# Performance work log

Hardware: AMD Instinct MI355X
Metric: run time of the kernel (lower is better)

The kernel has to match this reference:

```python
import jax, jax.numpy as jnp
import numpy as np
import math

RIEMANN_ZEROS_IM = (14.134725142, 21.022039639, 25.01085758, 30.424876126, 32.935061588,
    37.586178159, 40.918719012, 43.327073281, 48.005150881, 49.773832478, 52.970321478,
    56.446247697, 59.347044003, 60.831778525, 65.112544048, 67.079810529, 69.546401711,
    72.067157674, 75.704690699, 77.144840069, 79.33737502, 82.910380854, 84.735492981,
    87.425274613, 88.809111208, 92.491899271, 94.651344041, 95.870634228, 98.831194218,
    101.317851006, 103.72553804, 105.446623052)

D_MODEL = 1024
N_HEADS = 16
D_HEAD = D_MODEL // N_HEADS  # 64
N_PAIRS = D_HEAD // 2        # 32

# normalized inverse frequencies: gamma_n / gamma_1, inverted
_gamma = np.asarray(RIEMANN_ZEROS_IM[:N_PAIRS], dtype=np.float32)
INV_FREQ = jnp.asarray(1.0 / (_gamma / _gamma[0]))  # [n_pairs]


def _rotate(x, cos, sin):
    # x: [b,h,n,d_head]; cos/sin: [1,h,n,n_pairs]; interleaved pair rotation
    x1 = x[..., 0::2]
    x2 = x[..., 1::2]
    rx1 = x1 * cos - x2 * sin
    rx2 = x1 * sin + x2 * cos
    return jnp.stack([rx1, rx2], axis=-1).reshape(x.shape)


def setup_inputs() -> dict:
    key = jax.random.key(0)
    k1, k2, k3 = jax.random.split(key, 3)
    b, n = 4, 2048
    x = jax.random.normal(k1, (b, n, D_MODEL), dtype=jnp.float32)
    # torch Linear(d, 3d, bias=False): y = x @ W.T; we store W.T directly
    w_qkv = jax.random.normal(k2, (D_MODEL, 3 * D_MODEL), dtype=jnp.float32) / math.sqrt(D_MODEL)
    w_o = jax.random.normal(k3, (D_MODEL, D_MODEL), dtype=jnp.float32) / math.sqrt(D_MODEL)
    log_scale = jnp.zeros((N_HEADS,), dtype=jnp.float32)
    return {"x": x, "w_qkv": w_qkv, "w_o": w_o, "log_scale": log_scale}


def reference(x, w_qkv, w_o, log_scale):
    b, n, d = x.shape
    qkv = (x @ w_qkv).reshape(b, n, 3, N_HEADS, D_HEAD)
    q, k, v = qkv[:, :, 0], qkv[:, :, 1], qkv[:, :, 2]  # [b,n,h,dh]
    q = q.transpose(0, 2, 1, 3)  # [b,h,n,dh]
    k = k.transpose(0, 2, 1, 3)
    v = v.transpose(0, 2, 1, 3)

    scale = jnp.exp(log_scale)  # [h]
    pos = jnp.arange(n, dtype=jnp.float32)
    # theta: [1,h,n,n_pairs]
    theta = pos[None, None, :, None] * INV_FREQ[None, None, None, :] * scale[None, :, None, None]
    cos, sin = jnp.cos(theta), jnp.sin(theta)
    q = _rotate(q, cos, sin)
    k = _rotate(k, cos, sin)

    scores = jnp.einsum('bhqd,bhkd->bhqk', q, k) / math.sqrt(D_HEAD)
    causal = jnp.tril(jnp.ones((n, n), dtype=bool))
    scores = jnp.where(causal[None, None], scores, -jnp.inf)
    attn = jax.nn.softmax(scores, axis=-1)
    out = jnp.einsum('bhqk,bhkd->bhqd', attn, v)
    out = out.transpose(0, 2, 1, 3).reshape(b, n, d)
    return out @ w_o
```

## Files before the change

### kernel.cpp

```cpp
#include <hip/hip_runtime.h>
#include <hip/hip_bf16.h>

#define B_ 4
#define N_ 2048
#define DM 1024
#define NH 16
#define DH 64

typedef __attribute__((ext_vector_type(8))) __bf16 bf16x8;
typedef __attribute__((ext_vector_type(4))) float f32x4;
typedef __attribute__((ext_vector_type(4))) float float4v;
typedef __attribute__((ext_vector_type(4))) unsigned int uint4v;
typedef __attribute__((ext_vector_type(2))) unsigned int uint2v;
typedef __attribute__((ext_vector_type(4))) unsigned short ushort4v;

__device__ __forceinline__ float bf2f(unsigned short h) {
  union { unsigned int u; float f; } v; v.u = ((unsigned int)h) << 16; return v.f;
}
__device__ __forceinline__ unsigned short f2bf(float f) {
  __bf16 h = (__bf16)f;
  return __builtin_bit_cast(unsigned short, h);
}
__device__ __forceinline__ f32x4 mfma16(bf16x8 a, bf16x8 b, f32x4 c) {
  return __builtin_amdgcn_mfma_f32_16x16x32_bf16(a, b, c, 0, 0, 0);
}
__device__ __forceinline__ void gload_lds16(const void* g, void* l) {
  __builtin_amdgcn_global_load_lds(
      (const __attribute__((address_space(1))) unsigned int*)g,
      (__attribute__((address_space(3))) unsigned int*)l, 16, 0, 0);
}
__device__ __forceinline__ float fexp2(float x) {
  return __builtin_amdgcn_exp2f(x);
}

__constant__ float GAMMA_C[32] = {
  14.134725142f, 21.022039639f, 25.01085758f, 30.424876126f,
  32.935061588f, 37.586178159f, 40.918719012f, 43.327073281f,
  48.005150881f, 49.773832478f, 52.970321478f, 56.446247697f,
  59.347044003f, 60.831778525f, 65.112544048f, 67.079810529f,
  69.546401711f, 72.067157674f, 75.704690699f, 77.144840069f,
  79.33737502f,  82.910380854f, 84.735492981f, 87.425274613f,
  88.809111208f, 92.491899271f, 94.651344041f, 95.870634228f,
  98.831194218f, 101.317851006f, 103.72553804f, 105.446623052f
};

__global__ __launch_bounds__(256) void cast_f32_bf16(
    const float* __restrict__ in, unsigned short* __restrict__ out, int n4) {
  int i = blockIdx.x * 256 + threadIdx.x;
  if (i >= n4) return;
  float4v v = *(const float4v*)&in[(size_t)i * 4];
  ushort4v o;
  o[0] = f2bf(v[0]); o[1] = f2bf(v[1]); o[2] = f2bf(v[2]); o[3] = f2bf(v[3]);
  *(ushort4v*)&out[(size_t)i * 4] = o;
}

__global__ __launch_bounds__(256) void tcast(
    const float* __restrict__ in, unsigned short* __restrict__ out, int K, int N) {
  __shared__ float t[32][33];
  int n0 = blockIdx.x * 32, k0 = blockIdx.y * 32;
  int tx = threadIdx.x, ty = threadIdx.y;
#pragma unroll
  for (int j = 0; j < 4; ++j)
    t[ty + j * 8][tx] = in[(size_t)(k0 + ty + j * 8) * N + n0 + tx];
  __syncthreads();
#pragma unroll
  for (int j = 0; j < 4; ++j)
    out[(size_t)(n0 + ty + j * 8) * K + k0 + tx] = f2bf(t[tx][ty + j * 8]);
}

template <int OUTF32>
__global__ __launch_bounds__(256) void gemm_bt(
    const unsigned short* __restrict__ A, const unsigned short* __restrict__ BT,
    void* __restrict__ C, int M, int N, int K) {
  __shared__ unsigned short As[128 * 32];
  __shared__ unsigned short Bs[128 * 32];
  int tid = threadIdx.x;
  int lane = tid & 63, wid = tid >> 6;
  int wr = wid >> 1, wc = wid & 1;
  int lr = lane & 15, lg = lane >> 4;
  int bm = blockIdx.y * 128, bn = blockIdx.x * 128;
  int srow = lane >> 2, sch = lane & 3;
  f32x4 acc[4][4];
#pragma unroll
  for (int m = 0; m < 4; ++m)
#pragma unroll
    for (int n = 0; n < 4; ++n) acc[m][n] = (f32x4){0.f, 0.f, 0.f, 0.f};

  for (int k0 = 0; k0 < K; k0 += 32) {
    __syncthreads();
#pragma unroll
    for (int it = 0; it < 2; ++it) {
      int rbase = wid * 16 + it * 64;
      gload_lds16(&A[(size_t)(bm + rbase + srow) * K + k0 + sch * 8],
                  &As[rbase * 32]);
      gload_lds16(&BT[(size_t)(bn + rbase + srow) * K + k0 + sch * 8],
                  &Bs[rbase * 32]);
    }
    __syncthreads();
    bf16x8 af[4], bfr[4];
#pragma unroll
    for (int m = 0; m < 4; ++m)
      af[m] = *(const bf16x8*)&As[(wr * 64 + m * 16 + lr) * 32 + lg * 8];
#pragma unroll
    for (int n = 0; n < 4; ++n)
      bfr[n] = *(const bf16x8*)&Bs[(wc * 64 + n * 16 + lr) * 32 + lg * 8];
    __builtin_amdgcn_s_setprio(1);
#pragma unroll
    for (int m = 0; m < 4; ++m)
#pragma unroll
      for (int n = 0; n < 4; ++n)
        acc[m][n] = mfma16(af[m], bfr[n], acc[m][n]);
    __builtin_amdgcn_s_setprio(0);
  }
#pragma unroll
  for (int m = 0; m < 4; ++m)
#pragma unroll
    for (int n = 0; n < 4; ++n) {
      int row = bm + wr * 64 + m * 16 + lg * 4;
      int col = bn + wc * 64 + n * 16 + lr;
#pragma unroll
      for (int r = 0; r < 4; ++r) {
        if (OUTF32)
          ((float*)C)[(size_t)(row + r) * N + col] = acc[m][n][r];
        else
          ((unsigned short*)C)[(size_t)(row + r) * N + col] = f2bf(acc[m][n][r]);
      }
    }
}

__global__ __launch_bounds__(256) void rope_split(
    const unsigned short* __restrict__ qkv, const float* __restrict__ log_scale,
    unsigned short* __restrict__ Qr, unsigned short* __restrict__ Kr,
    unsigned short* __restrict__ Vr) {
  const float SC = 0.125f * 1.44269504089f;
  int t = blockIdx.x * 256 + threadIdx.x;
  int p = t & 31, h = (t >> 5) & 15, n = (t >> 9) & 2047, b = t >> 20;
  float invf = GAMMA_C[0] / GAMMA_C[p];
  float scale = __expf(log_scale[h]);
  float theta = ((float)n * invf) * scale;
  float sn, cs;
  sincosf(theta, &sn, &cs);
  size_t base = (size_t)(b * N_ + n) * (3 * DM) + h * DH + 2 * p;
  unsigned int qu = *(const unsigned int*)&qkv[base];
  unsigned int ku = *(const unsigned int*)&qkv[base + DM];
  unsigned int vu = *(const unsigned int*)&qkv[base + 2 * DM];
  float q1 = bf2f(qu & 0xffffu), q2 = bf2f(qu >> 16);
  float k1 = bf2f(ku & 0xffffu), k2 = bf2f(ku >> 16);
  unsigned int rq = (unsigned int)f2bf((q1 * cs - q2 * sn) * SC) |
                    ((unsigned int)f2bf((q1 * sn + q2 * cs) * SC) << 16);
  unsigned int rk = (unsigned int)f2bf(k1 * cs - k2 * sn) |
                    ((unsigned int)f2bf(k1 * sn + k2 * cs) << 16);
  size_t ob = (size_t)((b * NH + h) * N_ + n) * DH + 2 * p;
  *(unsigned int*)&Qr[ob] = rq;
  *(unsigned int*)&Kr[ob] = rk;
  *(unsigned int*)&Vr[ob] = vu;
}

__global__ __launch_bounds__(256) void attn_fwd(
    const unsigned short* __restrict__ Q, const unsigned short* __restrict__ K,
    const unsigned short* __restrict__ V, unsigned short* __restrict__ AO) {
  int orig = blockIdx.x;
  int wg = (orig & 7) * 128 + (orig >> 3);
  int i = wg & 15;
  int qt = ((wg >> 5) & 1) ? (15 - i) : i;
  int bh = wg >> 4;
  int b = bh >> 4, h = bh & 15;
  int q0 = qt * 128;
  int tid = threadIdx.x;
  int lane = tid & 63, w = tid >> 6;
  int lr = lane & 15, lg = lane >> 4;

  const unsigned short* Qh = Q + (size_t)bh * N_ * DH;
  const unsigned short* Kh = K + (size_t)bh * N_ * DH;
  const unsigned short* Vh = V + (size_t)bh * N_ * DH;

  __shared__ unsigned short Ks[64 * 64];
  __shared__ unsigned short Vt[64 * 64];
  __shared__ unsigned int PsU[4][32][32];

  bf16x8 qf[2][2];
#pragma unroll
  for (int m = 0; m < 2; ++m)
#pragma unroll
    for (int dh = 0; dh < 2; ++dh)
      qf[m][dh] = *(const bf16x8*)
          &Qh[(size_t)(q0 + w * 32 + m * 16 + lr) * DH + dh * 32 + lg * 8];

  f32x4 oacc[2][4];
#pragma unroll
  for (int m = 0; m < 2; ++m)
#pragma unroll
    for (int nb = 0; nb < 4; ++nb) oacc[m][nb] = (f32x4){0.f, 0.f, 0.f, 0.f};
  float mst[2] = {-1e30f, -1e30f};
  float lst[2] = {0.f, 0.f};

  int wkend = q0 + w * 32 + 31;
  int ksup = q0 + 128;
  int vch = tid & 7, vk = tid >> 3;
  int swz = 4 * (lr & 7);

  for (int k0 = 0; k0 < ksup; k0 += 64) {
    __syncthreads();
#pragma unroll
    for (int it = 0; it < 2; ++it) {
      int rbase = w * 8 + it * 32;
      int row = rbase + (lane >> 3);
      int sk = ((row & 7) ^ (row >> 3)) & 7;
      int ch = lane & 7;
      gload_lds16(&Kh[(size_t)(k0 + row) * DH + ((ch ^ sk) * 8)],
                  &Ks[rbase * 64]);
    }
#pragma unroll
    for (int it = 0; it < 2; ++it) {
      int k = vk + it * 32;
      uint4v vv = *(const uint4v*)&Vh[(size_t)(k0 + k) * DH + vch * 8];
      const unsigned short* pv = (const unsigned short*)&vv;
#pragma unroll
      for (int j = 0; j < 8; ++j) {
        int d = vch * 8 + j;
        int sv = (j ^ vch) & 7;
        Vt[d * 64 + (k ^ (sv << 3))] = pv[j];
      }
    }
    __syncthreads();
    if (k0 > wkend) continue;

    f32x4 s[2][4];
    __builtin_amdgcn_s_setprio(1);
#pragma unroll
    for (int nb = 0; nb < 4; ++nb) {
      int key = nb * 16 + lr;
      int sk = ((key & 7) ^ (key >> 3)) & 7;
      bf16x8 kf0 = *(const bf16x8*)&Ks[key * 64 + ((lg ^ sk) * 8)];
      bf16x8 kf1 = *(const bf16x8*)&Ks[key * 64 + (((4 + lg) ^ sk) * 8)];
#pragma unroll
      for (int m = 0; m < 2; ++m) {
        f32x4 z = (f32x4){0.f, 0.f, 0.f, 0.f};
        z = mfma16(kf0, qf[m][0], z);
        z = mfma16(kf1, qf[m][1], z);
        s[m][nb] = z;
      }
    }
    __builtin_amdgcn_s_setprio(0);

    float mx[2];
#pragma unroll
    for (int m = 0; m < 2; ++m) {
      int qm = q0 + w * 32 + m * 16;
      if (k0 + 63 > qm) {
        int q = qm + lr;
#pragma unroll
        for (int nb = 0; nb < 4; ++nb)
#pragma unroll
          for (int r = 0; r < 4; ++r)
            if (k0 + nb * 16 + lg * 4 + r > q) s[m][nb][r] = -1e30f;
      }
      float mx0 = fmaxf(fmaxf(s[m][0][0], s[m][0][1]),
                        fmaxf(s[m][0][2], s[m][0][3]));
      float mx1 = fmaxf(fmaxf(s[m][1][0], s[m][1][1]),
                        fmaxf(s[m][1][2], s[m][1][3]));
      float mx2 = fmaxf(fmaxf(s[m][2][0], s[m][2][1]),
                        fmaxf(s[m][2][2], s[m][2][3]));
      float mx3 = fmaxf(fmaxf(s[m][3][0], s[m][3][1]),
                        fmaxf(s[m][3][2], s[m][3][3]));
      float m01 = fmaxf(fmaxf(mx0, mx1), fmaxf(mx2, mx3));
      m01 = fmaxf(m01, __shfl_xor(m01, 16, 64));
      m01 = fmaxf(m01, __shfl_xor(m01, 32, 64));
      mx[m] = m01;
    }

    if (__any((mx[0] > mst[0] + 8.f) || (mx[1] > mst[1] + 8.f))) {
      float scs[2];
#pragma unroll
      for (int m = 0; m < 2; ++m) {
        float mnew = fmaxf(mst[m], mx[m]);
        float sc = fexp2(mst[m] - mnew);
        mst[m] = mnew;
        lst[m] *= sc;
        scs[m] = sc;
      }
#pragma unroll
      for (int m = 0; m < 2; ++m)
#pragma unroll
        for (int r = 0; r < 4; ++r) {
          float scr = __shfl(scs[m], lg * 4 + r, 64);
#pragma unroll
          for (int nb = 0; nb < 4; ++nb) oacc[m][nb][r] *= scr;
        }
    }

#pragma unroll
    for (int m = 0; m < 2; ++m) {
      float ps = 0.f;
      unsigned int pw[8];
#pragma unroll
      for (int nb = 0; nb < 4; ++nb)
#pragma unroll
        for (int rp = 0; rp < 2; ++rp) {
          float p0 = fexp2(s[m][nb][2 * rp] - mst[m]);
          float p1 = fexp2(s[m][nb][2 * rp + 1] - mst[m]);
          ps += p0 + p1;
          pw[nb * 2 + rp] =
              (unsigned int)f2bf(p0) | ((unsigned int)f2bf(p1) << 16);
        }
#pragma unroll
      for (int nb = 0; nb < 4; ++nb) {
        int c0 = (nb * 8 + lg * 2) ^ swz;
        *(uint2v*)&PsU[w][m * 16 + lr][c0] = (uint2v){pw[nb * 2], pw[nb * 2 + 1]};
      }
      ps += __shfl_xor(ps, 16, 64);
      ps += __shfl_xor(ps, 32, 64);
      lst[m] += ps;
    }
    asm volatile("s_waitcnt lgkmcnt(0)" ::: "memory");
    __builtin_amdgcn_sched_barrier(0);

    __builtin_amdgcn_s_setprio(1);
#pragma unroll
    for (int kh = 0; kh < 2; ++kh) {
      bf16x8 pf0 = *(const bf16x8*)&PsU[w][lr][(kh * 16 + lg * 4) ^ swz];
      bf16x8 pf1 = *(const bf16x8*)&PsU[w][16 + lr][(kh * 16 + lg * 4) ^ swz];
#pragma unroll
      for (int nb = 0; nb < 4; ++nb) {
        int d = nb * 16 + lr;
        int sv2 = ((d & 7) ^ (d >> 3)) & 7;
        bf16x8 vf = *(const bf16x8*)
            &Vt[d * 64 + ((kh * 32 + lg * 8) ^ (sv2 << 3))];
        oacc[0][nb] = mfma16(pf0, vf, oacc[0][nb]);
        oacc[1][nb] = mfma16(pf1, vf, oacc[1][nb]);
      }
    }
    __builtin_amdgcn_s_setprio(0);
  }

#pragma unroll
  for (int m = 0; m < 2; ++m) {
    float inv = 1.0f / lst[m];
#pragma unroll
    for (int r = 0; r < 4; ++r) {
      float invr = __shfl(inv, lg * 4 + r, 64);
      int q = q0 + w * 32 + m * 16 + lg * 4 + r;
#pragma unroll
      for (int nb = 0; nb < 4; ++nb) {
        float o = oacc[m][nb][r] * invr;
        AO[(size_t)(b * N_ + q) * DM + h * DH + nb * 16 + lr] = f2bf(o);
      }
    }
  }
}

extern "C" void kernel_launch(void* const* d_in, const int* in_sizes, int n_in,
                              void* d_out, int out_size, void* d_ws, size_t ws_size,
                              hipStream_t stream) {
  const float* x = (const float*)d_in[0];
  const float* w_qkv = (const float*)d_in[1];
  const float* w_o = (const float*)d_in[2];
  const float* log_scale = (const float*)d_in[3];
  float* out = (float*)d_out;

  char* ws = (char*)d_ws;
  unsigned short* xb  = (unsigned short*)(ws);
  unsigned short* ao  = xb;
  unsigned short* wqT = (unsigned short*)(ws + (16u << 20));
  unsigned short* woT = (unsigned short*)(ws + (22u << 20));
  unsigned short* qkv = (unsigned short*)(ws + (24u << 20));
  unsigned short* Qr  = (unsigned short*)(ws + (72u << 20));
  unsigned short* Kr  = (unsigned short*)(ws + (88u << 20));
  unsigned short* Vr  = (unsigned short*)(ws + (104u << 20));

  cast_f32_bf16<<<8192, 256, 0, stream>>>(x, xb, (B_ * N_ * DM) / 4);
  dim3 tb(32, 8);
  tcast<<<dim3(3 * DM / 32, DM / 32), tb, 0, stream>>>(w_qkv, wqT, DM, 3 * DM);
  tcast<<<dim3(DM / 32, DM / 32), tb, 0, stream>>>(w_o, woT, DM, DM);
  gemm_bt<0><<<dim3(3 * DM / 128, (B_ * N_) / 128), 256, 0, stream>>>(
      xb, wqT, qkv, B_ * N_, 3 * DM, DM);
  rope_split<<<(B_ * N_ * NH * 32) / 256, 256, 0, stream>>>(
      qkv, log_scale, Qr, Kr, Vr);
  attn_fwd<<<B_ * NH * (N_ / 128), 256, 0, stream>>>(Qr, Kr, Vr, ao);
  gemm_bt<1><<<dim3(DM / 128, (B_ * N_) / 128), 256, 0, stream>>>(
      ao, woT, out, B_ * N_, DM, DM);
}
```

Before: 246.0 us.

## Pre-transpose V in rope kernel and run attention as single-wave blocks without LDS staging

```diff
diff --git a/kernel.cpp b/kernel.cpp
--- a/kernel.cpp
+++ b/kernel.cpp
@@ -131,52 +131,71 @@
 __global__ __launch_bounds__(256) void rope_split(
     const unsigned short* __restrict__ qkv, const float* __restrict__ log_scale,
     unsigned short* __restrict__ Qr, unsigned short* __restrict__ Kr,
-    unsigned short* __restrict__ Vr) {
+    unsigned short* __restrict__ Vt) {
   const float SC = 0.125f * 1.44269504089f;
-  int t = blockIdx.x * 256 + threadIdx.x;
-  int p = t & 31, h = (t >> 5) & 15, n = (t >> 9) & 2047, b = t >> 20;
+  int nt = blockIdx.x, bh = blockIdx.y;
+  int b = bh >> 4, h = bh & 15;
+  int n0 = nt * 128;
+  int tid = threadIdx.x;
+  int p = tid & 31, nl0 = tid >> 5;
+  __shared__ unsigned int Vl[128][33];
   float invf = GAMMA_C[0] / GAMMA_C[p];
   float scale = __expf(log_scale[h]);
-  float theta = ((float)n * invf) * scale;
-  float sn, cs;
-  sincosf(theta, &sn, &cs);
-  size_t base = (size_t)(b * N_ + n) * (3 * DM) + h * DH + 2 * p;
-  unsigned int qu = *(const unsigned int*)&qkv[base];
-  unsigned int ku = *(const unsigned int*)&qkv[base + DM];
-  unsigned int vu = *(const unsigned int*)&qkv[base + 2 * DM];
-  float q1 = bf2f(qu & 0xffffu), q2 = bf2f(qu >> 16);
-  float k1 = bf2f(ku & 0xffffu), k2 = bf2f(ku >> 16);
-  unsigned int rq = (unsigned int)f2bf((q1 * cs - q2 * sn) * SC) |
-                    ((unsigned int)f2bf((q1 * sn + q2 * cs) * SC) << 16);
-  unsigned int rk = (unsigned int)f2bf(k1 * cs - k2 * sn) |
-                    ((unsigned int)f2bf(k1 * sn + k2 * cs) << 16);
-  size_t ob = (size_t)((b * NH + h) * N_ + n) * DH + 2 * p;
-  *(unsigned int*)&Qr[ob] = rq;
-  *(unsigned int*)&Kr[ob] = rk;
-  *(unsigned int*)&Vr[ob] = vu;
-}
-
-__global__ __launch_bounds__(256) void attn_fwd(
+#pragma unroll
+  for (int j = 0; j < 16; ++j) {
+    int nl = nl0 + j * 8;
+    int n = n0 + nl;
+    size_t base = (size_t)(b * N_ + n) * (3 * DM) + h * DH + 2 * p;
+    unsigned int qu = *(const unsigned int*)&qkv[base];
+    unsigned int ku = *(const unsigned int*)&qkv[base + DM];
+    unsigned int vu = *(const unsigned int*)&qkv[base + 2 * DM];
+    float th = (float)n * invf * scale;
+    float sn, cs;
+    sincosf(th, &sn, &cs);
+    float q1 = bf2f(qu & 0xffffu), q2 = bf2f(qu >> 16);
+    float k1 = bf2f(ku & 0xffffu), k2 = bf2f(ku >> 16);
+    unsigned int rq = (unsigned int)f2bf((q1 * cs - q2 * sn) * SC) |
+                      ((unsigned int)f2bf((q1 * sn + q2 * cs) * SC) << 16);
+    unsigned int rk = (unsigned int)f2bf(k1 * cs - k2 * sn) |
+                      ((unsigned int)f2bf(k1 * sn + k2 * cs) << 16);
+    size_t ob = (size_t)(bh * N_ + n) * DH + 2 * p;
+    *(unsigned int*)&Qr[ob] = rq;
+    *(unsigned int*)&Kr[ob] = rk;
+    Vl[nl][p] = vu;
+  }
+  __syncthreads();
+  int d = tid & 63, ch = tid >> 6;
+  int dp = d >> 1, sh = (d & 1) * 16;
+#pragma unroll
+  for (int j = 0; j < 4; ++j) {
+    int cc = ch + j * 4;
+    unsigned short o[8];
+#pragma unroll
+    for (int i = 0; i < 8; ++i)
+      o[i] = (unsigned short)(Vl[cc * 8 + i][dp] >> sh);
+    *(uint4v*)&Vt[(size_t)bh * DH * N_ + (size_t)d * N_ + n0 + cc * 8] =
+        *(const uint4v*)o;
+  }
+}
+
+__global__ __launch_bounds__(64) void attn_fwd(
     const unsigned short* __restrict__ Q, const unsigned short* __restrict__ K,
     const unsigned short* __restrict__ V, unsigned short* __restrict__ AO) {
   int orig = blockIdx.x;
-  int wg = (orig & 7) * 128 + (orig >> 3);
-  int i = wg & 15;
-  int qt = ((wg >> 5) & 1) ? (15 - i) : i;
-  int bh = wg >> 4;
+  int wg = (orig & 7) * 512 + (orig >> 3);
+  int bh = wg >> 6;
+  int raw = wg & 63;
+  int qt = (bh & 1) ? (63 - raw) : raw;
   int b = bh >> 4, h = bh & 15;
-  int q0 = qt * 128;
-  int tid = threadIdx.x;
-  int lane = tid & 63, w = tid >> 6;
+  int q0 = qt * 32;
+  int lane = threadIdx.x;
   int lr = lane & 15, lg = lane >> 4;
 
   const unsigned short* Qh = Q + (size_t)bh * N_ * DH;
   const unsigned short* Kh = K + (size_t)bh * N_ * DH;
-  const unsigned short* Vh = V + (size_t)bh * N_ * DH;
-
-  __shared__ unsigned short Ks[64 * 64];
-  __shared__ unsigned short Vt[64 * 64];
-  __shared__ unsigned int PsU[4][32][32];
+  const unsigned short* Vh = V + (size_t)bh * DH * N_;
+
+  __shared__ unsigned int PsU[32][32];
 
   bf16x8 qf[2][2];
 #pragma unroll
@@ -184,7 +203,7 @@
 #pragma unroll
     for (int dh = 0; dh < 2; ++dh)
       qf[m][dh] = *(const bf16x8*)
-          &Qh[(size_t)(q0 + w * 32 + m * 16 + lr) * DH + dh * 32 + lg * 8];
+          &Qh[(size_t)(q0 + m * 16 + lr) * DH + dh * 32 + lg * 8];
 
   f32x4 oacc[2][4];
 #pragma unroll
@@ -194,59 +213,40 @@
   float mst[2] = {-1e30f, -1e30f};
   float lst[2] = {0.f, 0.f};
 
-  int wkend = q0 + w * 32 + 31;
-  int ksup = q0 + 128;
-  int vch = tid & 7, vk = tid >> 3;
+  int wkend = q0 + 31;
   int swz = 4 * (lr & 7);
 
-  for (int k0 = 0; k0 < ksup; k0 += 64) {
-    __syncthreads();
-#pragma unroll
-    for (int it = 0; it < 2; ++it) {
-      int rbase = w * 8 + it * 32;
-      int row = rbase + (lane >> 3);
-      int sk = ((row & 7) ^ (row >> 3)) & 7;
-      int ch = lane & 7;
-      gload_lds16(&Kh[(size_t)(k0 + row) * DH + ((ch ^ sk) * 8)],
-                  &Ks[rbase * 64]);
-    }
-#pragma unroll
-    for (int it = 0; it < 2; ++it) {
-      int k = vk + it * 32;
-      uint4v vv = *(const uint4v*)&Vh[(size_t)(k0 + k) * DH + vch * 8];
-      const unsigned short* pv = (const unsigned short*)&vv;
-#pragma unroll
-      for (int j = 0; j < 8; ++j) {
-        int d = vch * 8 + j;
-        int sv = (j ^ vch) & 7;
-        Vt[d * 64 + (k ^ (sv << 3))] = pv[j];
-      }
-    }
-    __syncthreads();
-    if (k0 > wkend) continue;
-
+  for (int k0 = 0; k0 <= wkend; k0 += 64) {
+    bf16x8 kf0[4], kf1[4];
+#pragma unroll
+    for (int nb = 0; nb < 4; ++nb) {
+      size_t krow = (size_t)(k0 + nb * 16 + lr) * DH;
+      kf0[nb] = *(const bf16x8*)&Kh[krow + lg * 8];
+      kf1[nb] = *(const bf16x8*)&Kh[krow + 32 + lg * 8];
+    }
     f32x4 s[2][4];
     __builtin_amdgcn_s_setprio(1);
 #pragma unroll
-    for (int nb = 0; nb < 4; ++nb) {
-      int key = nb * 16 + lr;
-      int sk = ((key & 7) ^ (key >> 3)) & 7;
-      bf16x8 kf0 = *(const bf16x8*)&Ks[key * 64 + ((lg ^ sk) * 8)];
-      bf16x8 kf1 = *(const bf16x8*)&Ks[key * 64 + (((4 + lg) ^ sk) * 8)];
+    for (int nb = 0; nb < 4; ++nb)
 #pragma unroll
       for (int m = 0; m < 2; ++m) {
         f32x4 z = (f32x4){0.f, 0.f, 0.f, 0.f};
-        z = mfma16(kf0, qf[m][0], z);
-        z = mfma16(kf1, qf[m][1], z);
+        z = mfma16(kf0[nb], qf[m][0], z);
+        z = mfma16(kf1[nb], qf[m][1], z);
         s[m][nb] = z;
       }
-    }
     __builtin_amdgcn_s_setprio(0);
 
+    bf16x8 vf0[4];
+#pragma unroll
+    for (int nb = 0; nb < 4; ++nb)
+      vf0[nb] = *(const bf16x8*)
+          &Vh[(size_t)(nb * 16 + lr) * N_ + k0 + lg * 8];
+
     float mx[2];
 #pragma unroll
     for (int m = 0; m < 2; ++m) {
-      int qm = q0 + w * 32 + m * 16;
+      int qm = q0 + m * 16;
       if (k0 + 63 > qm) {
         int q = qm + lr;
 #pragma unroll
@@ -306,7 +306,7 @@
 #pragma unroll
       for (int nb = 0; nb < 4; ++nb) {
         int c0 = (nb * 8 + lg * 2) ^ swz;
-        *(uint2v*)&PsU[w][m * 16 + lr][c0] = (uint2v){pw[nb * 2], pw[nb * 2 + 1]};
+        *(uint2v*)&PsU[m * 16 + lr][c0] = (uint2v){pw[nb * 2], pw[nb * 2 + 1]};
       }
       ps += __shfl_xor(ps, 16, 64);
       ps += __shfl_xor(ps, 32, 64);
@@ -316,21 +316,32 @@
     __builtin_amdgcn_sched_barrier(0);
 
     __builtin_amdgcn_s_setprio(1);
-#pragma unroll
-    for (int kh = 0; kh < 2; ++kh) {
-      bf16x8 pf0 = *(const bf16x8*)&PsU[w][lr][(kh * 16 + lg * 4) ^ swz];
-      bf16x8 pf1 = *(const bf16x8*)&PsU[w][16 + lr][(kh * 16 + lg * 4) ^ swz];
+    {
+      bf16x8 pf0 = *(const bf16x8*)&PsU[lr][(lg * 4) ^ swz];
+      bf16x8 pf1 = *(const bf16x8*)&PsU[16 + lr][(lg * 4) ^ swz];
 #pragma unroll
       for (int nb = 0; nb < 4; ++nb) {
-        int d = nb * 16 + lr;
-        int sv2 = ((d & 7) ^ (d >> 3)) & 7;
-        bf16x8 vf = *(const bf16x8*)
-            &Vt[d * 64 + ((kh * 32 + lg * 8) ^ (sv2 << 3))];
-        oacc[0][nb] = mfma16(pf0, vf, oacc[0][nb]);
-        oacc[1][nb] = mfma16(pf1, vf, oacc[1][nb]);
+        oacc[0][nb] = mfma16(pf0, vf0[nb], oacc[0][nb]);
+        oacc[1][nb] = mfma16(pf1, vf0[nb], oacc[1][nb]);
       }
     }
     __builtin_amdgcn_s_setprio(0);
+    {
+      bf16x8 vf1[4];
+#pragma unroll
+      for (int nb = 0; nb < 4; ++nb)
+        vf1[nb] = *(const bf16x8*)
+            &Vh[(size_t)(nb * 16 + lr) * N_ + k0 + 32 + lg * 8];
+      bf16x8 pf0 = *(const bf16x8*)&PsU[lr][(16 + lg * 4) ^ swz];
+      bf16x8 pf1 = *(const bf16x8*)&PsU[16 + lr][(16 + lg * 4) ^ swz];
+      __builtin_amdgcn_s_setprio(1);
+#pragma unroll
+      for (int nb = 0; nb < 4; ++nb) {
+        oacc[0][nb] = mfma16(pf0, vf1[nb], oacc[0][nb]);
+        oacc[1][nb] = mfma16(pf1, vf1[nb], oacc[1][nb]);
+      }
+      __builtin_amdgcn_s_setprio(0);
+    }
   }
 
 #pragma unroll
@@ -339,7 +350,7 @@
 #pragma unroll
     for (int r = 0; r < 4; ++r) {
       float invr = __shfl(inv, lg * 4 + r, 64);
-      int q = q0 + w * 32 + m * 16 + lg * 4 + r;
+      int q = q0 + m * 16 + lg * 4 + r;
 #pragma unroll
       for (int nb = 0; nb < 4; ++nb) {
         float o = oacc[m][nb][r] * invr;
@@ -366,7 +377,7 @@
   unsigned short* qkv = (unsigned short*)(ws + (24u << 20));
   unsigned short* Qr  = (unsigned short*)(ws + (72u << 20));
   unsigned short* Kr  = (unsigned short*)(ws + (88u << 20));
-  unsigned short* Vr  = (unsigned short*)(ws + (104u << 20));
+  unsigned short* Vt  = (unsigned short*)(ws + (104u << 20));
 
   cast_f32_bf16<<<8192, 256, 0, stream>>>(x, xb, (B_ * N_ * DM) / 4);
   dim3 tb(32, 8);
@@ -374,9 +385,9 @@
   tcast<<<dim3(DM / 32, DM / 32), tb, 0, stream>>>(w_o, woT, DM, DM);
   gemm_bt<0><<<dim3(3 * DM / 128, (B_ * N_) / 128), 256, 0, stream>>>(
       xb, wqT, qkv, B_ * N_, 3 * DM, DM);
-  rope_split<<<(B_ * N_ * NH * 32) / 256, 256, 0, stream>>>(
-      qkv, log_scale, Qr, Kr, Vr);
-  attn_fwd<<<B_ * NH * (N_ / 128), 256, 0, stream>>>(Qr, Kr, Vr, ao);
+  rope_split<<<dim3(16, B_ * NH), 256, 0, stream>>>(
+      qkv, log_scale, Qr, Kr, Vt);
+  attn_fwd<<<B_ * NH * (N_ / 32), 64, 0, stream>>>(Qr, Kr, Vt, ao);
   gemm_bt<1><<<dim3(DM / 128, (B_ * N_) / 128), 256, 0, stream>>>(
       ao, woT, out, B_ * N_, DM, DM);
 }
```

After: 284.1 us. +15.5%, slower.

## Add 256x256-tile 8-wave GEMM with swizzled LDS and XCD remap for QKV projection

Applied to the files above, without the earlier changes.

```diff
diff --git a/kernel.cpp b/kernel.cpp
--- a/kernel.cpp
+++ b/kernel.cpp
@@ -125,6 +125,128 @@
         else
           ((unsigned short*)C)[(size_t)(row + r) * N + col] = f2bf(acc[m][n][r]);
       }
+    }
+}
+
+__global__ __launch_bounds__(512) void gemm256(
+    const unsigned short* __restrict__ A, const unsigned short* __restrict__ BT,
+    unsigned short* __restrict__ C, int M, int N, int K) {
+  extern __shared__ unsigned short smem[];
+  unsigned short* Asb = smem;
+  unsigned short* Bsb = smem + 32768;
+  int tid = threadIdx.x;
+  int lane = tid & 63, w = tid >> 6;
+  int wr = w >> 2, wc = w & 3;
+  int lr = lane & 15, lg = lane >> 4;
+  int nbx = N >> 8;
+  int cpx = gridDim.x >> 3;
+  int orig = blockIdx.x;
+  int wg = (orig & 7) * cpx + (orig >> 3);
+  int bm = (wg / nbx) << 8, bn = (wg % nbx) << 8;
+  int srow = lane >> 3, sch = lane & 7;
+
+  f32x4 acc[8][4];
+#pragma unroll
+  for (int m = 0; m < 8; ++m)
+#pragma unroll
+    for (int n = 0; n < 4; ++n) acc[m][n] = (f32x4){0.f, 0.f, 0.f, 0.f};
+
+  auto STAGE = [&](int buf, int t) {
+    int k0 = t << 6;
+#pragma unroll
+    for (int it = 0; it < 4; ++it) {
+      int rbase = w * 32 + it * 8;
+      int row = rbase + srow;
+      int sk = row & 7;
+      gload_lds16(&A[(size_t)(bm + row) * K + k0 + ((sch ^ sk) * 8)],
+                  &Asb[buf * 16384 + rbase * 64]);
+      gload_lds16(&BT[(size_t)(bn + row) * K + k0 + ((sch ^ sk) * 8)],
+                  &Bsb[buf * 16384 + rbase * 64]);
+    }
+  };
+
+  int NT = K >> 6;
+  STAGE(0, 0);
+  STAGE(1, 1);
+  asm volatile("s_waitcnt vmcnt(8)" ::: "memory");
+  __builtin_amdgcn_s_barrier();
+
+  bf16x8 a[4][2], b[4][2];
+  int cur = 0;
+  for (int t = 0; t < NT; ++t) {
+    const unsigned short* Ab = &Asb[cur * 16384];
+    const unsigned short* Bb = &Bsb[cur * 16384];
+
+#define RD_A(half)                                                         \
+  {                                                                        \
+    _Pragma("unroll") for (int m4 = 0; m4 < 4; ++m4) {                     \
+      int ra = wr * 128 + (half) * 64 + m4 * 16 + lr;                      \
+      _Pragma("unroll") for (int kk = 0; kk < 2; ++kk)                     \
+          a[m4][kk] = *(const bf16x8*)                                     \
+              &Ab[ra * 64 + (((kk * 4 + lg) ^ (ra & 7)) * 8)];             \
+    }                                                                      \
+  }
+#define RD_B(half)                                                         \
+  {                                                                        \
+    _Pragma("unroll") for (int n2 = 0; n2 < 2; ++n2) {                     \
+      int n = (half) * 2 + n2;                                             \
+      int rb = wc * 64 + n * 16 + lr;                                      \
+      _Pragma("unroll") for (int kk = 0; kk < 2; ++kk)                     \
+          b[n][kk] = *(const bf16x8*)                                      \
+              &Bb[rb * 64 + (((kk * 4 + lg) ^ (rb & 7)) * 8)];             \
+    }                                                                      \
+  }
+#define WAITL                                                              \
+  asm volatile("s_waitcnt lgkmcnt(0)" ::: "memory");                       \
+  __builtin_amdgcn_sched_barrier(0);
+#define MM(mh, nh)                                                         \
+  __builtin_amdgcn_s_setprio(1);                                           \
+  _Pragma("unroll") for (int m4 = 0; m4 < 4; ++m4)                         \
+      _Pragma("unroll") for (int n2 = 0; n2 < 2; ++n2)                     \
+          _Pragma("unroll") for (int kk = 0; kk < 2; ++kk)                 \
+              acc[(mh) * 4 + m4][(nh) * 2 + n2] =                          \
+                  mfma16(a[m4][kk], b[(nh) * 2 + n2][kk],                  \
+                         acc[(mh) * 4 + m4][(nh) * 2 + n2]);               \
+  __builtin_amdgcn_s_setprio(0);
+
+    RD_A(0); RD_B(0);
+    __builtin_amdgcn_s_barrier();
+    WAITL; MM(0, 0);
+    __builtin_amdgcn_s_barrier();
+    RD_B(1);
+    __builtin_amdgcn_s_barrier();
+    WAITL; MM(0, 1);
+    __builtin_amdgcn_s_barrier();
+    RD_A(1);
+    __builtin_amdgcn_s_barrier();
+    WAITL; MM(1, 0);
+    __builtin_amdgcn_s_barrier();
+    MM(1, 1);
+    __builtin_amdgcn_s_barrier();
+
+    if (t + 2 < NT) {
+      STAGE(cur, t + 2);
+      asm volatile("s_waitcnt vmcnt(8)" ::: "memory");
+    } else if (t + 1 < NT) {
+      asm volatile("s_waitcnt vmcnt(0)" ::: "memory");
+    }
+    __builtin_amdgcn_s_barrier();
+    cur ^= 1;
+  }
+#undef RD_A
+#undef RD_B
+#undef WAITL
+#undef MM
+
+#pragma unroll
+  for (int m = 0; m < 8; ++m)
+#pragma unroll
+    for (int n = 0; n < 4; ++n) {
+      int row = bm + wr * 128 + m * 16 + lg * 4;
+      int col = bn + wc * 64 + n * 16 + lr;
+#pragma unroll
+      for (int r = 0; r < 4; ++r)
+        C[(size_t)(row + r) * N + col] = f2bf(acc[m][n][r]);
     }
 }
 
@@ -368,11 +490,14 @@
   unsigned short* Kr  = (unsigned short*)(ws + (88u << 20));
   unsigned short* Vr  = (unsigned short*)(ws + (104u << 20));
 
+  hipFuncSetAttribute((const void*)gemm256,
+                      hipFuncAttributeMaxDynamicSharedMemorySize, 131072);
+
   cast_f32_bf16<<<8192, 256, 0, stream>>>(x, xb, (B_ * N_ * DM) / 4);
   dim3 tb(32, 8);
   tcast<<<dim3(3 * DM / 32, DM / 32), tb, 0, stream>>>(w_qkv, wqT, DM, 3 * DM);
   tcast<<<dim3(DM / 32, DM / 32), tb, 0, stream>>>(w_o, woT, DM, DM);
-  gemm_bt<0><<<dim3(3 * DM / 128, (B_ * N_) / 128), 256, 0, stream>>>(
+  gemm256<<<(B_ * N_ / 256) * (3 * DM / 256), 512, 131072, stream>>>(
       xb, wqT, qkv, B_ * N_, 3 * DM, DM);
   rope_split<<<(B_ * N_ * NH * 32) / 256, 256, 0, stream>>>(
       qkv, log_scale, Qr, Kr, Vr);
```

Result: slower. 252.5 us (+2.7%).

## Double-buffer K tiles, prefetch V from qkv, drop V copy in rope

Applied to the files above, without the earlier changes.

```diff
diff --git a/kernel.cpp b/kernel.cpp
--- a/kernel.cpp
+++ b/kernel.cpp
@@ -130,8 +130,7 @@
 
 __global__ __launch_bounds__(256) void rope_split(
     const unsigned short* __restrict__ qkv, const float* __restrict__ log_scale,
-    unsigned short* __restrict__ Qr, unsigned short* __restrict__ Kr,
-    unsigned short* __restrict__ Vr) {
+    unsigned short* __restrict__ Qr, unsigned short* __restrict__ Kr) {
   const float SC = 0.125f * 1.44269504089f;
   int t = blockIdx.x * 256 + threadIdx.x;
   int p = t & 31, h = (t >> 5) & 15, n = (t >> 9) & 2047, b = t >> 20;
@@ -143,7 +142,6 @@
   size_t base = (size_t)(b * N_ + n) * (3 * DM) + h * DH + 2 * p;
   unsigned int qu = *(const unsigned int*)&qkv[base];
   unsigned int ku = *(const unsigned int*)&qkv[base + DM];
-  unsigned int vu = *(const unsigned int*)&qkv[base + 2 * DM];
   float q1 = bf2f(qu & 0xffffu), q2 = bf2f(qu >> 16);
   float k1 = bf2f(ku & 0xffffu), k2 = bf2f(ku >> 16);
   unsigned int rq = (unsigned int)f2bf((q1 * cs - q2 * sn) * SC) |
@@ -153,12 +151,11 @@
   size_t ob = (size_t)((b * NH + h) * N_ + n) * DH + 2 * p;
   *(unsigned int*)&Qr[ob] = rq;
   *(unsigned int*)&Kr[ob] = rk;
-  *(unsigned int*)&Vr[ob] = vu;
-}
-
-__global__ __launch_bounds__(256) void attn_fwd(
+}
+
+__global__ __launch_bounds__(256, 4) void attn_fwd(
     const unsigned short* __restrict__ Q, const unsigned short* __restrict__ K,
-    const unsigned short* __restrict__ V, unsigned short* __restrict__ AO) {
+    const unsigned short* __restrict__ qkv, unsigned short* __restrict__ AO) {
   int orig = blockIdx.x;
   int wg = (orig & 7) * 128 + (orig >> 3);
   int i = wg & 15;
@@ -172,9 +169,9 @@
 
   const unsigned short* Qh = Q + (size_t)bh * N_ * DH;
   const unsigned short* Kh = K + (size_t)bh * N_ * DH;
-  const unsigned short* Vh = V + (size_t)bh * N_ * DH;
-
-  __shared__ unsigned short Ks[64 * 64];
+  const unsigned short* Vq = qkv + (size_t)b * N_ * (3 * DM) + 2 * DM + h * DH;
+
+  __shared__ unsigned short Ks[2][64 * 64];
   __shared__ unsigned short Vt[64 * 64];
   __shared__ unsigned int PsU[4][32][32];
 
@@ -199,138 +196,163 @@
   int vch = tid & 7, vk = tid >> 3;
   int swz = 4 * (lr & 7);
 
-  for (int k0 = 0; k0 < ksup; k0 += 64) {
-    __syncthreads();
+  auto KSTAGE = [&](int buf, int kk0) {
 #pragma unroll
     for (int it = 0; it < 2; ++it) {
       int rbase = w * 8 + it * 32;
       int row = rbase + (lane >> 3);
       int sk = ((row & 7) ^ (row >> 3)) & 7;
       int ch = lane & 7;
-      gload_lds16(&Kh[(size_t)(k0 + row) * DH + ((ch ^ sk) * 8)],
-                  &Ks[rbase * 64]);
-    }
-#pragma unroll
-    for (int it = 0; it < 2; ++it) {
-      int k = vk + it * 32;
-      uint4v vv = *(const uint4v*)&Vh[(size_t)(k0 + k) * DH + vch * 8];
-      const unsigned short* pv = (const unsigned short*)&vv;
-#pragma unroll
-      for (int j = 0; j < 8; ++j) {
-        int d = vch * 8 + j;
-        int sv = (j ^ vch) & 7;
-        Vt[d * 64 + (k ^ (sv << 3))] = pv[j];
-      }
-    }
+      gload_lds16(&Kh[(size_t)(kk0 + row) * DH + ((ch ^ sk) * 8)],
+                  &Ks[buf][rbase * 64]);
+    }
+  };
+  auto VWRITE = [&](uint4v v0, uint4v v1) {
+    const unsigned short* p0 = (const unsigned short*)&v0;
+    const unsigned short* p1 = (const unsigned short*)&v1;
+#pragma unroll
+    for (int j = 0; j < 8; ++j) {
+      int d = vch * 8 + j;
+      int sv = (j ^ vch) & 7;
+      Vt[d * 64 + (vk ^ (sv << 3))] = p0[j];
+      Vt[d * 64 + ((vk + 32) ^ (sv << 3))] = p1[j];
+    }
+  };
+
+  {
+    uint4v v0 = *(const uint4v*)&Vq[(size_t)vk * (3 * DM) + vch * 8];
+    uint4v v1 = *(const uint4v*)&Vq[(size_t)(vk + 32) * (3 * DM) + vch * 8];
+    KSTAGE(0, 0);
+    VWRITE(v0, v1);
     __syncthreads();
-    if (k0 > wkend) continue;
-
-    f32x4 s[2][4];
-    __builtin_amdgcn_s_setprio(1);
-#pragma unroll
-    for (int nb = 0; nb < 4; ++nb) {
-      int key = nb * 16 + lr;
-      int sk = ((key & 7) ^ (key >> 3)) & 7;
-      bf16x8 kf0 = *(const bf16x8*)&Ks[key * 64 + ((lg ^ sk) * 8)];
-      bf16x8 kf1 = *(const bf16x8*)&Ks[key * 64 + (((4 + lg) ^ sk) * 8)];
+  }
+  int cur = 0;
+
+  for (int k0 = 0; k0 < ksup; k0 += 64) {
+    bool hn = (k0 + 64 < ksup);
+    uint4v nv0, nv1;
+    if (hn) {
+      nv0 = *(const uint4v*)&Vq[(size_t)(k0 + 64 + vk) * (3 * DM) + vch * 8];
+      nv1 = *(const uint4v*)&Vq[(size_t)(k0 + 96 + vk) * (3 * DM) + vch * 8];
+      KSTAGE(cur ^ 1, k0 + 64);
+    }
+
+    if (k0 <= wkend) {
+      f32x4 s[2][4];
+      __builtin_amdgcn_s_setprio(1);
+#pragma unroll
+      for (int nb = 0; nb < 4; ++nb) {
+        int key = nb * 16 + lr;
+        int sk = ((key & 7) ^ (key >> 3)) & 7;
+        bf16x8 kf0 = *(const bf16x8*)&Ks[cur][key * 64 + ((lg ^ sk) * 8)];
+        bf16x8 kf1 = *(const bf16x8*)&Ks[cur][key * 64 + (((4 + lg) ^ sk) * 8)];
+#pragma unroll
+        for (int m = 0; m < 2; ++m) {
+          f32x4 z = (f32x4){0.f, 0.f, 0.f, 0.f};
+          z = mfma16(kf0, qf[m][0], z);
+          z = mfma16(kf1, qf[m][1], z);
+          s[m][nb] = z;
+        }
+      }
+      __builtin_amdgcn_s_setprio(0);
+
+      float mx[2];
 #pragma unroll
       for (int m = 0; m < 2; ++m) {
-        f32x4 z = (f32x4){0.f, 0.f, 0.f, 0.f};
-        z = mfma16(kf0, qf[m][0], z);
-        z = mfma16(kf1, qf[m][1], z);
-        s[m][nb] = z;
-      }
-    }
-    __builtin_amdgcn_s_setprio(0);
-
-    float mx[2];
-#pragma unroll
-    for (int m = 0; m < 2; ++m) {
-      int qm = q0 + w * 32 + m * 16;
-      if (k0 + 63 > qm) {
-        int q = qm + lr;
+        int qm = q0 + w * 32 + m * 16;
+        if (k0 + 63 > qm) {
+          int q = qm + lr;
+#pragma unroll
+          for (int nb = 0; nb < 4; ++nb)
+#pragma unroll
+            for (int r = 0; r < 4; ++r)
+              if (k0 + nb * 16 + lg * 4 + r > q) s[m][nb][r] = -1e30f;
+        }
+        float mx0 = fmaxf(fmaxf(s[m][0][0], s[m][0][1]),
+                          fmaxf(s[m][0][2], s[m][0][3]));
+        float mx1 = fmaxf(fmaxf(s[m][1][0], s[m][1][1]),
+                          fmaxf(s[m][1][2], s[m][1][3]));
+        float mx2 = fmaxf(fmaxf(s[m][2][0], s[m][2][1]),
+                          fmaxf(s[m][2][2], s[m][2][3]));
+        float mx3 = fmaxf(fmaxf(s[m][3][0], s[m][3][1]),
+                          fmaxf(s[m][3][2], s[m][3][3]));
+        float m01 = fmaxf(fmaxf(mx0, mx1), fmaxf(mx2, mx3));
+        m01 = fmaxf(m01, __shfl_xor(m01, 16, 64));
+        m01 = fmaxf(m01, __shfl_xor(m01, 32, 64));
+        mx[m] = m01;
+      }
+
+      if (__any((mx[0] > mst[0] + 8.f) || (mx[1] > mst[1] + 8.f))) {
+        float scs[2];
+#pragma unroll
+        for (int m = 0; m < 2; ++m) {
+          float mnew = fmaxf(mst[m], mx[m]);
+          float sc = fexp2(mst[m] - mnew);
+          mst[m] = mnew;
+          lst[m] *= sc;
+          scs[m] = sc;
+        }
+#pragma unroll
+        for (int m = 0; m < 2; ++m)
+#pragma unroll
+          for (int r = 0; r < 4; ++r) {
+            float scr = __shfl(scs[m], lg * 4 + r, 64);
+#pragma unroll
+            for (int nb = 0; nb < 4; ++nb) oacc[m][nb][r] *= scr;
+          }
+      }
+
+#pragma unroll
+      for (int m = 0; m < 2; ++m) {
+        float ps = 0.f;
+        unsigned int pw[8];
 #pragma unroll
         for (int nb = 0; nb < 4; ++nb)
 #pragma unroll
-          for (int r = 0; r < 4; ++r)
-            if (k0 + nb * 16 + lg * 4 + r > q) s[m][nb][r] = -1e30f;
-      }
-      float mx0 = fmaxf(fmaxf(s[m][0][0], s[m][0][1]),
-                        fmaxf(s[m][0][2], s[m][0][3]));
-      float mx1 = fmaxf(fmaxf(s[m][1][0], s[m][1][1]),
-                        fmaxf(s[m][1][2], s[m][1][3]));
-      float mx2 = fmaxf(fmaxf(s[m][2][0], s[m][2][1]),
-                        fmaxf(s[m][2][2], s[m][2][3]));
-      float mx3 = fmaxf(fmaxf(s[m][3][0], s[m][3][1]),
-                        fmaxf(s[m][3][2], s[m][3][3]));
-      float m01 = fmaxf(fmaxf(mx0, mx1), fmaxf(mx2, mx3));
-      m01 = fmaxf(m01, __shfl_xor(m01, 16, 64));
-      m01 = fmaxf(m01, __shfl_xor(m01, 32, 64));
-      mx[m] = m01;
-    }
-
-    if (__any((mx[0] > mst[0] + 8.f) || (mx[1] > mst[1] + 8.f))) {
-      float scs[2];
-#pragma unroll
-      for (int m = 0; m < 2; ++m) {
-        float mnew = fmaxf(mst[m], mx[m]);
-        float sc = fexp2(mst[m] - mnew);
-        mst[m] = mnew;
-        lst[m] *= sc;
-        scs[m] = sc;
-      }
-#pragma unroll
-      for (int m = 0; m < 2; ++m)
-#pragma unroll
-        for (int r = 0; r < 4; ++r) {
-          float scr = __shfl(scs[m], lg * 4 + r, 64);
-#pragma unroll
-          for (int nb = 0; nb < 4; ++nb) oacc[m][nb][r] *= scr;
+          for (int rp = 0; rp < 2; ++rp) {
+            float p0 = fexp2(s[m][nb][2 * rp] - mst[m]);
+            float p1 = fexp2(s[m][nb][2 * rp + 1] - mst[m]);
+            ps += p0 + p1;
+            pw[nb * 2 + rp] =
+                (unsigned int)f2bf(p0) | ((unsigned int)f2bf(p1) << 16);
+          }
+#pragma unroll
+        for (int nb = 0; nb < 4; ++nb) {
+          int c0 = (nb * 8 + lg * 2) ^ swz;
+          *(uint2v*)&PsU[w][m * 16 + lr][c0] =
+              (uint2v){pw[nb * 2], pw[nb * 2 + 1]};
         }
-    }
-
-#pragma unroll
-    for (int m = 0; m < 2; ++m) {
-      float ps = 0.f;
-      unsigned int pw[8];
-#pragma unroll
-      for (int nb = 0; nb < 4; ++nb)
-#pragma unroll
-        for (int rp = 0; rp < 2; ++rp) {
-          float p0 = fexp2(s[m][nb][2 * rp] - mst[m]);
-          float p1 = fexp2(s[m][nb][2 * rp + 1] - mst[m]);
-          ps += p0 + p1;
-          pw[nb * 2 + rp] =
-              (unsigned int)f2bf(p0) | ((unsigned int)f2bf(p1) << 16);
+        ps += __shfl_xor(ps, 16, 64);
+        ps += __shfl_xor(ps, 32, 64);
+        lst[m] += ps;
+      }
+      asm volatile("s_waitcnt lgkmcnt(0)" ::: "memory");
+      __builtin_amdgcn_sched_barrier(0);
+
+      __builtin_amdgcn_s_setprio(1);
+#pragma unroll
+      for (int kh = 0; kh < 2; ++kh) {
+        bf16x8 pf0 = *(const bf16x8*)&PsU[w][lr][(kh * 16 + lg * 4) ^ swz];
+        bf16x8 pf1 = *(const bf16x8*)&PsU[w][16 + lr][(kh * 16 + lg * 4) ^ swz];
+#pragma unroll
+        for (int nb = 0; nb < 4; ++nb) {
+          int d = nb * 16 + lr;
+          int sv2 = ((d & 7) ^ (d >> 3)) & 7;
+          bf16x8 vf = *(const bf16x8*)
+              &Vt[d * 64 + ((kh * 32 + lg * 8) ^ (sv2 << 3))];
+          oacc[0][nb] = mfma16(pf0, vf, oacc[0][nb]);
+          oacc[1][nb] = mfma16(pf1, vf, oacc[1][nb]);
         }
-#pragma unroll
-      for (int nb = 0; nb < 4; ++nb) {
-        int c0 = (nb * 8 + lg * 2) ^ swz;
-        *(uint2v*)&PsU[w][m * 16 + lr][c0] = (uint2v){pw[nb * 2], pw[nb * 2 + 1]};
-      }
-      ps += __shfl_xor(ps, 16, 64);
-      ps += __shfl_xor(ps, 32, 64);
-      lst[m] += ps;
-    }
-    asm volatile("s_waitcnt lgkmcnt(0)" ::: "memory");
-    __builtin_amdgcn_sched_barrier(0);
-
-    __builtin_amdgcn_s_setprio(1);
-#pragma unroll
-    for (int kh = 0; kh < 2; ++kh) {
-      bf16x8 pf0 = *(const bf16x8*)&PsU[w][lr][(kh * 16 + lg * 4) ^ swz];
-      bf16x8 pf1 = *(const bf16x8*)&PsU[w][16 + lr][(kh * 16 + lg * 4) ^ swz];
-#pragma unroll
-      for (int nb = 0; nb < 4; ++nb) {
-        int d = nb * 16 + lr;
-        int sv2 = ((d & 7) ^ (d >> 3)) & 7;
-        bf16x8 vf = *(const bf16x8*)
-            &Vt[d * 64 + ((kh * 32 + lg * 8) ^ (sv2 << 3))];
-        oacc[0][nb] = mfma16(pf0, vf, oacc[0][nb]);
-        oacc[1][nb] = mfma16(pf1, vf, oacc[1][nb]);
-      }
-    }
-    __builtin_amdgcn_s_setprio(0);
+      }
+      __builtin_amdgcn_s_setprio(0);
+    }
+
+    __syncthreads();
+    if (hn) {
+      VWRITE(nv0, nv1);
+      __syncthreads();
+    }
+    cur ^= 1;
   }
 
 #pragma unroll
@@ -366,7 +388,6 @@
   unsigned short* qkv = (unsigned short*)(ws + (24u << 20));
   unsigned short* Qr  = (unsigned short*)(ws + (72u << 20));
   unsigned short* Kr  = (unsigned short*)(ws + (88u << 20));
-  unsigned short* Vr  = (unsigned short*)(ws + (104u << 20));
 
   cast_f32_bf16<<<8192, 256, 0, stream>>>(x, xb, (B_ * N_ * DM) / 4);
   dim3 tb(32, 8);
@@ -375,8 +396,8 @@
   gemm_bt<0><<<dim3(3 * DM / 128, (B_ * N_) / 128), 256, 0, stream>>>(
       xb, wqT, qkv, B_ * N_, 3 * DM, DM);
   rope_split<<<(B_ * N_ * NH * 32) / 256, 256, 0, stream>>>(
-      qkv, log_scale, Qr, Kr, Vr);
-  attn_fwd<<<B_ * NH * (N_ / 128), 256, 0, stream>>>(Qr, Kr, Vr, ao);
+      qkv, log_scale, Qr, Kr);
+  attn_fwd<<<B_ * NH * (N_ / 128), 256, 0, stream>>>(Qr, Kr, qkv, ao);
   gemm_bt<1><<<dim3(DM / 128, (B_ * N_) / 128), 256, 0, stream>>>(
       ao, woT, out, B_ * N_, DM, DM);
 }
```

Result: slower. 418.7 us (+70.2%).
